# Optimization experiments

Measured on AMD Instinct MI355X. Metric: run time of the kernel, lower is better.

## Reference

```python
import jax, jax.numpy as jnp
import numpy as np

B, T, NA, NV, K, SD, H, E = 128, 64, 10, 16, 4, 512, 256, 32

def _lin(key, fan_in, fan_out):
    k1, k2 = jax.random.split(key)
    s = 1.0 / np.sqrt(fan_in)
    W = jax.random.uniform(k1, (fan_in, fan_out), jnp.float32, -s, s)
    b = jax.random.uniform(k2, (fan_out,), jnp.float32, -s, s)
    return W, b

def setup_inputs() -> dict:
    key = jax.random.key(0)
    ks = jax.random.split(key, 16)
    inp = {
        "qvals": jax.random.normal(ks[0], (B, T, NA), jnp.float32),
        "causal_relations": jax.random.randint(ks[1], (B, T, K, NV), 0, NA, jnp.int32),
        "states": jax.random.normal(ks[2], (B, T, SD), jnp.float32),
    }
    inp["w00_l1_W"], inp["w00_l1_b"] = _lin(ks[3], SD + NV, H)
    inp["w00_l2_W"], inp["w00_l2_b"] = _lin(ks[4], H, K)
    inp["b00_W"], inp["b00_b"] = _lin(ks[5], SD + NV, 1)
    inp["w01_W"], inp["w01_b"] = _lin(ks[6], SD, NA)
    inp["b01_W"], inp["b01_b"] = _lin(ks[7], SD, 1)
    inp["w1_l1_W"], inp["w1_l1_b"] = _lin(ks[8], SD, H)
    inp["w1_l2_W"], inp["w1_l2_b"] = _lin(ks[9], H, (NV + 1) * E)
    inp["b1_W"], inp["b1_b"] = _lin(ks[10], SD, E)
    inp["w2_l1_W"], inp["w2_l1_b"] = _lin(ks[11], SD, H)
    inp["w2_l2_W"], inp["w2_l2_b"] = _lin(ks[12], H, E)
    inp["b2_l1_W"], inp["b2_l1_b"] = _lin(ks[13], SD, E)
    inp["b2_l2_W"], inp["b2_l2_b"] = _lin(ks[14], E, 1)
    return inp

def reference(qvals, causal_relations, states,
              w00_l1_W, w00_l1_b, w00_l2_W, w00_l2_b, b00_W, b00_b,
              w01_W, w01_b, b01_W, b01_b,
              w1_l1_W, w1_l1_b, w1_l2_W, w1_l2_b, b1_W, b1_b,
              w2_l1_W, w2_l1_b, w2_l2_W, w2_l2_b,
              b2_l1_W, b2_l1_b, b2_l2_W, b2_l2_b):
    b, t, na = qvals.shape
    nv = causal_relations.shape[-1]
    sd = states.shape[-1]
    emb = b1_W.shape[1]

    # (b,t,k,nv) -> (b,t,nv,k); gather per-variable selected agent q-values
    cr = jnp.swapaxes(causal_relations, 2, 3)
    gathered = jnp.take_along_axis(qvals[:, :, None, :], cr, axis=-1)  # (b,t,nv,k)

    # Per-variable hypernets. Original builds a one-hot over n_variables but sets
    # var_onehot[variable] = 1, i.e. batch row `variable` becomes all-ones
    # (replicated faithfully). Split the first Linear into state part + onehot part:
    h_base = states @ w00_l1_W[:sd] + w00_l1_b   # (b,t,H)
    h_delta = w00_l1_W[sd:].sum(0)               # (H,)  contribution of all-ones onehot row
    g_base = states @ b00_W[:sd] + b00_b         # (b,t,1)
    g_delta = b00_W[sd:].sum(0)                  # (1,)

    def per_var(v):
        h = jax.nn.relu(h_base.at[v].add(h_delta))
        w0 = h @ w00_l2_W + w00_l2_b             # (b,t,k)
        b0 = g_base.at[v].add(g_delta)[..., 0]   # (b,t)
        return w0, b0

    w00, b00v = jax.vmap(per_var)(jnp.arange(nv))  # (nv,b,t,k), (nv,b,t)

    # group_qval_v = gathered_v @ |w0_v| + b0_v
    group = jnp.einsum('btvk,vbtk->btv', gathered, jnp.abs(w00)) + jnp.moveaxis(b00v, 0, -1)

    # residual agent mix (hyper_w0_1 / hyper_b0_1): plain linear hypernet, no abs in source
    w01 = states @ w01_W + w01_b                 # (b,t,na)
    other = jnp.einsum('bta,bta->bt', qvals, w01) + (states @ b01_W + b01_b)[..., 0]
    gq = jnp.concatenate([group, other[..., None]], axis=-1)  # (b,t,nv+1)

    # QMIX-style two-layer mix with hypernet weights
    w1 = jnp.abs((jax.nn.relu(states @ w1_l1_W + w1_l1_b) @ w1_l2_W + w1_l2_b)
                 .reshape(b, t, nv + 1, emb))
    b1 = states @ b1_W + b1_b                    # (b,t,E)
    hidden = jax.nn.elu(jnp.einsum('btv,btve->bte', gq, w1) + b1)
    w2 = jnp.abs(jax.nn.relu(states @ w2_l1_W + w2_l1_b) @ w2_l2_W + w2_l2_b)  # (b,t,E)
    b2 = jax.nn.relu(states @ b2_l1_W + b2_l1_b) @ b2_l2_W + b2_l2_b           # (b,t,1)
    y = jnp.sum(hidden * w2, axis=-1, keepdims=True) + b2
    return y  # (b,t,1)
```

## Files before the change

### kernel.cpp

```cpp
#include <hip/hip_runtime.h>
#include <hip/hip_bf16.h>


typedef __hip_bfloat16 bf16;
typedef unsigned short ushort_t;
typedef __attribute__((ext_vector_type(8))) short short8;
typedef __attribute__((ext_vector_type(4))) float f32x4;

#define PA_OFF 0
#define PA_TILES 56
#define PB_OFF (PA_TILES * 16 * 64 * 8 * 2)
#define PB_TILES 36
#define FB_OFF (PB_OFF + PB_TILES * 8 * 64 * 8 * 2)
#define NCST 2854
#define WS_NEED (size_t)(FB_OFF + NCST * 4 + 32)

#define MFMA16(a, b, c) __builtin_amdgcn_mfma_f32_16x16x32_bf16(a, b, c, 0, 0, 0)

__device__ __forceinline__ float us2f(ushort_t x) {
  unsigned u = ((unsigned)x) << 16; float f; __builtin_memcpy(&f, &u, 4); return f;
}
__device__ __forceinline__ ushort_t f2us(float v) {
  bf16 h = __float2bfloat16(v); ushort_t r; __builtin_memcpy(&r, &h, 2); return r;
}
template <bool F32>
__device__ __forceinline__ float LD(const void* p, size_t i) {
  if (F32) return ((const float*)p)[i];
  return us2f(((const ushort_t*)p)[i]);
}

__device__ __forceinline__ int detect_f32(const void* states) {
  const unsigned short* u = (const unsigned short*)states;
  int lane = threadIdx.x & 63;
  int bad = 0;
  for (int i = lane; i < 512; i += 64) {
    unsigned short x = u[i];
    int e = (x >> 7) & 0xFF;
    if (e > 140 || (((x & 0x7FFFu) != 0) && e < 100)) bad++;
  }
  for (int off = 32; off; off >>= 1) bad += __shfl_down(bad, off);
  return __shfl(bad, 0) > 20;
}

__device__ __forceinline__ void pa_store(ushort_t* pa, int np, int k, ushort_t v) {
  int t = np >> 4, lm = np & 15, ks = k >> 5, qq = (k >> 3) & 3, j = k & 7;
  pa[(size_t)t * 8192 + ks * 512 + (qq * 16 + lm) * 8 + j] = v;
}
__device__ __forceinline__ void pb_store(ushort_t* pb, int np, int k, ushort_t v) {
  int t = np >> 4, lm = np & 15, ks = k >> 5, qq = (k >> 3) & 3, j = k & 7;
  pb[(size_t)t * 4096 + ks * 512 + (qq * 16 + lm) * 8 + j] = v;
}

template <bool F32>
__device__ void prep_body(int gtid, int T, char* ws,
    const void* w00l1W, const void* w00l1b, const void* w00l2W, const void* w00l2b,
    const void* b00W, const void* b00b,
    const void* w01W, const void* w01b, const void* b01W, const void* b01b,
    const void* w1l1W, const void* w1l1b, const void* w1l2W, const void* w1l2b,
    const void* b1W, const void* b1b,
    const void* w2l1W, const void* w2l1b, const void* w2l2W, const void* w2l2b,
    const void* b2l1W, const void* b2l1b, const void* b2l2W, const void* b2l2b) {
  ushort_t* pa = (ushort_t*)(ws + PA_OFF);
  ushort_t* pb = (ushort_t*)(ws + PB_OFF);
  float* cst = (float*)(ws + FB_OFF);
  for (int i = gtid; i < 131072; i += T) {
    int k = i >> 8, n = i & 255;
    pa_store(pa, n, k, f2us(LD<F32>(w1l1W, i)));
    pa_store(pa, 256 + n, k, f2us(LD<F32>(w2l1W, i)));
    pa_store(pa, 512 + n, k, f2us(LD<F32>(w00l1W, i)));
  }
  for (int i = gtid; i < 16384; i += T) {
    int k = i >> 5, n = i & 31;
    pa_store(pa, 768 + n, k, f2us(LD<F32>(b1W, i)));
    pa_store(pa, 800 + n, k, f2us(LD<F32>(b2l1W, i)));
  }
  for (int i = gtid; i < 5120; i += T) {
    int k = i / 10, n = i % 10;
    pa_store(pa, 832 + n, k, f2us(LD<F32>(w01W, i)));
  }
  for (int i = gtid; i < 512; i += T) {
    pa_store(pa, 842, i, f2us(LD<F32>(b00W, i)));
    pa_store(pa, 843, i, f2us(LD<F32>(b01W, i)));
  }
  for (int z = gtid; z < 2048; z += T) {
    int ks = z >> 7, qq = (z >> 5) & 3, lm = 12 + ((z >> 3) & 3), j = z & 7;
    pa[(size_t)52 * 8192 + ks * 512 + (qq * 16 + lm) * 8 + j] = 0;
  }
  for (int i = gtid; i < 139264; i += T) {
    int k = i / 544, n = i % 544;
    pb_store(pb, n, k, f2us(LD<F32>(w1l2W, i)));
  }
  for (int i = gtid; i < 8192; i += T) {
    int k = i >> 5, n = i & 31;
    pb_store(pb, 544 + n, k, f2us(LD<F32>(w2l2W, i)));
  }
  for (int i = gtid; i < NCST; i += T) {
    float x;
    if (i < 896) {
      int c = i;
      if (c < 256) x = LD<F32>(w1l1b, c);
      else if (c < 512) x = LD<F32>(w2l1b, c - 256);
      else if (c < 768) x = LD<F32>(w00l1b, c - 512);
      else if (c < 800) x = LD<F32>(b1b, c - 768);
      else if (c < 832) x = LD<F32>(b2l1b, c - 800);
      else if (c < 842) x = LD<F32>(w01b, c - 832);
      else if (c == 842) x = LD<F32>(b00b, 0);
      else if (c == 843) x = LD<F32>(b01b, 0);
      else x = 0.f;
    } else if (i < 1536) {
      int c = i - 896;
      x = (c < 544) ? LD<F32>(w1l2b, c) : (c < 576 ? LD<F32>(w2l2b, c - 544) : 0.f);
    } else if (i < 1792) {
      int j = i - 1536; float s = 0.f;
      for (int z = 0; z < 16; ++z) s += LD<F32>(w00l1W, (size_t)(512 + z) * 256 + j);
      x = s;
    } else if (i < 2816) x = LD<F32>(w00l2W, i - 1792);
    else if (i < 2820) x = LD<F32>(w00l2b, i - 2816);
    else if (i < 2852) x = LD<F32>(b2l2W, i - 2820);
    else if (i == 2852) x = LD<F32>(b2l2b, 0);
    else { float s = 0.f; for (int z = 0; z < 16; ++z) s += LD<F32>(b00W, 512 + z); x = s; }
    cst[i] = x;
  }
}

__global__ __launch_bounds__(256) void prep_kernel(char* ws, const void* states,
    const void* w00l1W, const void* w00l1b, const void* w00l2W, const void* w00l2b,
    const void* b00W, const void* b00b,
    const void* w01W, const void* w01b, const void* b01W, const void* b01b,
    const void* w1l1W, const void* w1l1b, const void* w1l2W, const void* w1l2b,
    const void* b1W, const void* b1b,
    const void* w2l1W, const void* w2l1b, const void* w2l2W, const void* w2l2b,
    const void* b2l1W, const void* b2l1b, const void* b2l2W, const void* b2l2b) {
  int gtid = blockIdx.x * 256 + threadIdx.x;
  int T = gridDim.x * 256;
  if (detect_f32(states))
    prep_body<true>(gtid, T, ws, w00l1W, w00l1b, w00l2W, w00l2b, b00W, b00b,
        w01W, w01b, b01W, b01b, w1l1W, w1l1b, w1l2W, w1l2b, b1W, b1b,
        w2l1W, w2l1b, w2l2W, w2l2b, b2l1W, b2l1b, b2l2W, b2l2b);
  else
    prep_body<false>(gtid, T, ws, w00l1W, w00l1b, w00l2W, w00l2b, b00W, b00b,
        w01W, w01b, b01W, b01b, w1l1W, w1l1b, w1l2W, w1l2b, b1W, b1b,
        w2l1W, w2l1b, w2l2W, w2l2b, b2l1W, b2l1b, b2l2W, b2l2b);
}

struct SmemM {
  union {
    __align__(16) ushort_t sA[2][8192];
    __align__(16) ushort_t w1a[32][544];
  } u;
  __align__(16) ushort_t Am1[2][4096];
  __align__(16) ushort_t Am2[2][4096];
  __align__(16) ushort_t hb[32][264];
  float hd[256];
  float w2l[1024];
  float b1v[32][32];
  float rbv[32][32];
  float w2v[32][32];
  float w01v[32][12];
  float qv[32][10];
  unsigned char cr[32][64];
  float w0c[32][4], w0s[32][4];
  float gq[32][18];
  float gbv[32], b01v[32];
  float hid[32][33];
};

template <bool F32>
__device__ void mixer_body(SmemM& sm, const char* ws, int n0,
    const void* qvals, const int* crel, const void* states, void* out) {
  const int tid = threadIdx.x;
  const int lane = tid & 63, wv = tid >> 6;
  const int q = lane >> 4, lm = lane & 15;
  const int b_blk = n0 >> 6;
  const ushort_t* pa = (const ushort_t*)(ws + PA_OFF);
  const ushort_t* pb = (const ushort_t*)(ws + PB_OFF);
  const float* cstg = (const float*)(ws + FB_OFF);

  int sidx[7]; bool sreal[7];
#pragma unroll
  for (int i = 0; i < 7; ++i) {
    int s = wv + 8 * i;
    sreal[i] = (s < 53);
    sidx[i] = sreal[i] ? s : wv;
  }
  const ushort_t* baseA = pa + lane * 8;

  short8 curA[7];
  if (F32) {
    f32x4 va[8];
#pragma unroll
    for (int it = 0; it < 4; ++it) {
      int fi = tid + it * 512;
      int ln = fi & 63, ks = (fi >> 6) & 15, G = fi >> 10;
      int row = G * 16 + (ln & 15), col = ks * 32 + (ln >> 4) * 8;
      const f32x4* p = (const f32x4*)((const float*)states + (size_t)(n0 + row) * 512 + col);
      va[2 * it] = p[0];
      va[2 * it + 1] = p[1];
    }
#pragma unroll
    for (int i = 0; i < 7; ++i) curA[i] = *(const short8*)(baseA + (size_t)sidx[i] * 8192);
#pragma unroll
    for (int it = 0; it < 4; ++it) {
      int fi = tid + it * 512;
      int ln = fi & 63, ks = (fi >> 6) & 15, G = fi >> 10;
      f32x4 v0 = va[2 * it], v1 = va[2 * it + 1];
      ushort_t v[8];
      v[0] = f2us(v0[0]); v[1] = f2us(v0[1]); v[2] = f2us(v0[2]); v[3] = f2us(v0[3]);
      v[4] = f2us(v1[0]); v[5] = f2us(v1[1]); v[6] = f2us(v1[2]); v[7] = f2us(v1[3]);
      *(short8*)&sm.u.sA[G][(size_t)(ks * 64 + ln) * 8] = *(short8*)v;
    }
  } else {
    short8 vb[2];
#pragma unroll
    for (int it = 0; it < 2; ++it) {
      int fi = tid + it * 512;
      int ln = fi & 63, ks = (fi >> 6) & 15, G = fi >> 10;
      int row = G * 16 + (ln & 15), col = ks * 32 + (ln >> 4) * 8;
      vb[it] = *(const short8*)((const ushort_t*)states + (size_t)(n0 + row) * 512 + col);
    }
#pragma unroll
    for (int i = 0; i < 7; ++i) curA[i] = *(const short8*)(baseA + (size_t)sidx[i] * 8192);
#pragma unroll
    for (int it = 0; it < 2; ++it) {
      int fi = tid + it * 512;
      int ln = fi & 63, ks = (fi >> 6) & 15, G = fi >> 10;
      *(short8*)&sm.u.sA[G][(size_t)(ks * 64 + ln) * 8] = vb[it];
    }
  }
  for (int i = tid; i < 320; i += 512) sm.qv[i / 10][i % 10] = LD<F32>(qvals, (size_t)(n0 + i / 10) * 10 + i % 10);
  for (int i = tid; i < 2048; i += 512) sm.cr[i >> 6][i & 63] = (unsigned char)crel[(size_t)n0 * 64 + i];
  if (tid < 256) sm.hd[tid] = cstg[1536 + tid];
  for (int i = tid; i < 1024; i += 512) sm.w2l[i] = cstg[1792 + i];
  __syncthreads();

  {
    f32x4 accA[7][2];
#pragma unroll
    for (int i = 0; i < 7; ++i) { accA[i][0] = (f32x4){0,0,0,0}; accA[i][1] = (f32x4){0,0,0,0}; }
    short8 nxt[7];
#pragma unroll
    for (int ks = 0; ks < 16; ++ks) {
      if (ks < 15) {
#pragma unroll
        for (int i = 0; i < 7; ++i)
          nxt[i] = *(const short8*)(baseA + (size_t)sidx[i] * 8192 + (ks + 1) * 512);
      }
      short8 a0 = *(const short8*)&sm.u.sA[0][(ks * 64 + lane) * 8];
      short8 a1 = *(const short8*)&sm.u.sA[1][(ks * 64 + lane) * 8];
#pragma unroll
      for (int i = 0; i < 7; ++i) {
        accA[i][0] = MFMA16(a0, curA[i], accA[i][0]);
        accA[i][1] = MFMA16(a1, curA[i], accA[i][1]);
      }
#pragma unroll
      for (int i = 0; i < 7; ++i) curA[i] = nxt[i];
    }
#pragma unroll
    for (int i = 0; i < 7; ++i) {
      if (!sreal[i]) continue;
      int c = sidx[i] * 16 + lm;
      if (c >= 844) continue;
      float bias = cstg[c];
      int ks2 = (c & 255) >> 5, q2 = (c >> 3) & 3, j2 = c & 7;
#pragma unroll
      for (int G = 0; G < 2; ++G) {
        f32x4 acc = accA[i][G];
        int rb = G * 16 + q * 4;
        if (c < 256) {
#pragma unroll
          for (int g = 0; g < 4; ++g) {
            float v = acc[g] + bias;
            sm.Am1[G][(ks2 * 64 + q2 * 16 + q * 4 + g) * 8 + j2] = f2us(v > 0.f ? v : 0.f);
          }
        } else if (c < 512) {
#pragma unroll
          for (int g = 0; g < 4; ++g) {
            float v = acc[g] + bias;
            sm.Am2[G][(ks2 * 64 + q2 * 16 + q * 4 + g) * 8 + j2] = f2us(v > 0.f ? v : 0.f);
          }
        } else if (c < 768) {
#pragma unroll
          for (int g = 0; g < 4; ++g) sm.hb[rb + g][c - 512] = f2us(acc[g] + bias);
        } else if (c < 800) {
#pragma unroll
          for (int g = 0; g < 4; ++g) sm.b1v[rb + g][c - 768] = acc[g] + bias;
        } else if (c < 832) {
#pragma unroll
          for (int g = 0; g < 4; ++g) { float v = acc[g] + bias; sm.rbv[rb + g][c - 800] = v > 0.f ? v : 0.f; }
        } else if (c < 842) {
#pragma unroll
          for (int g = 0; g < 4; ++g) sm.w01v[rb + g][c - 832] = acc[g] + bias;
        } else if (c == 842) {
#pragma unroll
          for (int g = 0; g < 4; ++g) sm.gbv[rb + g] = acc[g] + bias;
        } else {
#pragma unroll
          for (int g = 0; g < 4; ++g) sm.b01v[rb + g] = acc[g] + bias;
        }
      }
    }
  }

  int tix[5]; bool treal[5];
#pragma unroll
  for (int i = 0; i < 5; ++i) {
    int t = wv + 8 * i;
    treal[i] = (t < 36);
    tix[i] = treal[i] ? t : wv;
  }
  const ushort_t* baseB = pb + lane * 8;
  short8 curB[5];
#pragma unroll
  for (int i = 0; i < 5; ++i) curB[i] = *(const short8*)(baseB + (size_t)tix[i] * 4096);
  __syncthreads();

  {
    f32x4 accB[5][2];
#pragma unroll
    for (int i = 0; i < 5; ++i) { accB[i][0] = (f32x4){0,0,0,0}; accB[i][1] = (f32x4){0,0,0,0}; }
    short8 nxt[5];
#pragma unroll
    for (int ks = 0; ks < 8; ++ks) {
      if (ks < 7) {
#pragma unroll
        for (int i = 0; i < 5; ++i)
          nxt[i] = *(const short8*)(baseB + (size_t)tix[i] * 4096 + (ks + 1) * 512);
      }
      short8 m1a0 = *(const short8*)&sm.Am1[0][(ks * 64 + lane) * 8];
      short8 m1a1 = *(const short8*)&sm.Am1[1][(ks * 64 + lane) * 8];
      short8 m2a0 = *(const short8*)&sm.Am2[0][(ks * 64 + lane) * 8];
      short8 m2a1 = *(const short8*)&sm.Am2[1][(ks * 64 + lane) * 8];
#pragma unroll
      for (int i = 0; i < 5; ++i) {
        short8 x0 = (tix[i] < 34) ? m1a0 : m2a0;
        short8 x1 = (tix[i] < 34) ? m1a1 : m2a1;
        accB[i][0] = MFMA16(x0, curB[i], accB[i][0]);
        accB[i][1] = MFMA16(x1, curB[i], accB[i][1]);
      }
#pragma unroll
      for (int i = 0; i < 5; ++i) curB[i] = nxt[i];
    }
#pragma unroll
    for (int i = 0; i < 5; ++i) {
      if (!treal[i]) continue;
      int c = tix[i] * 16 + lm;
      float bias = cstg[896 + c];
#pragma unroll
      for (int G = 0; G < 2; ++G) {
        f32x4 acc = accB[i][G];
        int rb = G * 16 + q * 4;
        if (c < 544) {
#pragma unroll
          for (int g = 0; g < 4; ++g) sm.u.w1a[rb + g][c] = f2us(fabsf(acc[g] + bias));
        } else {
          int e = c - 544;
#pragma unroll
          for (int g = 0; g < 4; ++g) sm.w2v[rb + g][e] = fabsf(acc[g] + bias);
        }
      }
    }
  }
  __syncthreads();

  if (tid < 256) {
    int r = tid >> 3, k = (tid >> 1) & 3, sflag = tid & 1;
    float a = 0.f;
    for (int j = 0; j < 256; ++j) {
      float h = us2f(sm.hb[r][j]);
      if (sflag) h += sm.hd[j];
      h = h > 0.f ? h : 0.f;
      a = fmaf(h, sm.w2l[j * 4 + k], a);
    }
    a += cstg[2816 + k];
    if (sflag) sm.w0s[r][k] = a; else sm.w0c[r][k] = a;
  }
  __syncthreads();

  {
    int r = tid >> 4, v = tid & 15;
    bool sp = (v == b_blk);
    const float* w0 = sp ? sm.w0s[r] : sm.w0c[r];
    float g = sm.gbv[r] + (sp ? cstg[2853] : 0.f);
#pragma unroll
    for (int k = 0; k < 4; ++k) {
      int a = sm.cr[r][k * 16 + v];
      g = fmaf(sm.qv[r][a], fabsf(w0[k]), g);
    }
    sm.gq[r][v] = g;
  }
  if (tid < 32) {
    float o = sm.b01v[tid];
#pragma unroll
    for (int a = 0; a < 10; ++a) o = fmaf(sm.qv[tid][a], sm.w01v[tid][a], o);
    sm.gq[tid][16] = o;
  }
  __syncthreads();

  for (int p = tid; p < 1024; p += 512) {
    int r = p >> 5, e = p & 31;
    float h = sm.b1v[r][e];
#pragma unroll
    for (int v = 0; v < 17; ++v) h = fmaf(sm.gq[r][v], us2f(sm.u.w1a[r][v * 32 + e]), h);
    float hid = h > 0.f ? h : (expf(h) - 1.f);
    sm.hid[r][e] = hid * sm.w2v[r][e] + sm.rbv[r][e] * cstg[2820 + e];
  }
  __syncthreads();

  if (tid < 32) {
    float y = cstg[2852];
#pragma unroll
    for (int e = 0; e < 32; ++e) y += sm.hid[tid][e];
    if (F32) ((float*)out)[n0 + tid] = y;
    else ((bf16*)out)[n0 + tid] = __float2bfloat16(y);
  }
}

__global__ __launch_bounds__(512, 2) void causal_mixer_mfma(const char* ws,
    const void* qvals, const int* crel, const void* states, void* out) {
  __shared__ SmemM sm;
  int n0 = blockIdx.x * 32;
  if (detect_f32(states))
    mixer_body<true>(sm, ws, n0, qvals, crel, states, out);
  else
    mixer_body<false>(sm, ws, n0, qvals, crel, states, out);
}

struct SmemF {
  float s[16][516]; float buf[16][258]; float hd[256];
  float q[16][10]; int cr[16][66];
  float w0c[16][4], w0s[16][4]; float gq[16][17];
  float w01[16][10]; float b01[16]; float gb[16]; float gd;
  float hid[16][32]; float w2[16][32]; float rb[16][32];
};

template <bool F32>
__device__ void fb_body(SmemF& sm, int tid, int n0, int b_blk,
    const void* qvals, const int* crel, const void* states,
    const void* w00l1W, const void* w00l1b, const void* w00l2W, const void* w00l2b,
    const void* b00W, const void* b00b,
    const void* w01W, const void* w01b, const void* b01W, const void* b01b,
    const void* w1l1W, const void* w1l1b, const void* w1l2W, const void* w1l2b,
    const void* b1W, const void* b1b,
    const void* w2l1W, const void* w2l1b, const void* w2l2W, const void* w2l2b,
    const void* b2l1W, const void* b2l1b, const void* b2l2W, const void* b2l2b,
    void* out) {
  for (int idx = tid; idx < 16 * 512; idx += 256) {
    int r = idx >> 9, i = idx & 511;
    sm.s[r][i] = LD<F32>(states, (size_t)(n0 + r) * 512 + i);
  }
  for (int idx = tid; idx < 160; idx += 256) {
    int r = idx / 10, a = idx % 10;
    sm.q[r][a] = LD<F32>(qvals, (size_t)(n0 + r) * 10 + a);
  }
  for (int idx = tid; idx < 16 * 64; idx += 256) {
    int r = idx >> 6, kv = idx & 63;
    sm.cr[r][kv] = crel[(size_t)(n0 + r) * 64 + kv];
  }
  if (tid == 0) {
    float gd = 0.f;
    for (int i = 512; i < 528; ++i) gd += LD<F32>(b00W, i);
    sm.gd = gd;
  }
  __syncthreads();
  {
    const int j = tid;
    float hd = 0.f;
    for (int i = 0; i < 16; ++i) hd += LD<F32>(w00l1W, (size_t)(512 + i) * 256 + j);
    sm.hd[j] = hd;
    float acc[16]; float bj = LD<F32>(w00l1b, j);
#pragma unroll
    for (int r = 0; r < 16; ++r) acc[r] = bj;
    for (int i = 0; i < 512; ++i) {
      float w = LD<F32>(w00l1W, (size_t)i * 256 + j);
#pragma unroll
      for (int r = 0; r < 16; ++r) acc[r] = fmaf(sm.s[r][i], w, acc[r]);
    }
#pragma unroll
    for (int r = 0; r < 16; ++r) sm.buf[r][j] = acc[r];
  }
  __syncthreads();
  if (tid < 64) {
    int r = tid >> 2, k = tid & 3;
    float aC = 0.f, aS = 0.f;
    for (int j = 0; j < 256; ++j) {
      float hb = sm.buf[r][j];
      float w = LD<F32>(w00l2W, j * 4 + k);
      float hc = hb > 0.f ? hb : 0.f;
      float hbs = hb + sm.hd[j];
      float hsv = hbs > 0.f ? hbs : 0.f;
      aC = fmaf(hc, w, aC); aS = fmaf(hsv, w, aS);
    }
    float bk = LD<F32>(w00l2b, k);
    sm.w0c[r][k] = aC + bk; sm.w0s[r][k] = aS + bk;
  } else if (tid < 224) {
    int p = tid - 64; int r = p / 10, a = p % 10;
    float acc = 0.f;
    for (int i = 0; i < 512; ++i) acc = fmaf(sm.s[r][i], LD<F32>(w01W, (size_t)i * 10 + a), acc);
    sm.w01[r][a] = acc + LD<F32>(w01b, a);
  } else if (tid < 240) {
    int r = tid - 224;
    float acc = 0.f;
    for (int i = 0; i < 512; ++i) acc = fmaf(sm.s[r][i], LD<F32>(b00W, i), acc);
    sm.gb[r] = acc + LD<F32>(b00b, 0);
  } else {
    int r = tid - 240;
    float acc = 0.f;
    for (int i = 0; i < 512; ++i) acc = fmaf(sm.s[r][i], LD<F32>(b01W, i), acc);
    sm.b01[r] = acc + LD<F32>(b01b, 0);
  }
  __syncthreads();
  {
    int r = tid >> 4, v = tid & 15;
    bool sp = (v == b_blk);
    const float* w0 = sp ? sm.w0s[r] : sm.w0c[r];
    float g = sm.gb[r] + (sp ? sm.gd : 0.f);
#pragma unroll
    for (int k = 0; k < 4; ++k) {
      int a = sm.cr[r][k * 16 + v];
      g = fmaf(sm.q[r][a], fabsf(w0[k]), g);
    }
    sm.gq[r][v] = g;
  }
  if (tid < 16) {
    int r = tid;
    float o = sm.b01[r];
    for (int a = 0; a < 10; ++a) o = fmaf(sm.q[r][a], sm.w01[r][a], o);
    sm.gq[r][16] = o;
  }
  __syncthreads();
  {
    const int j = tid;
    float acc[16]; float bj = LD<F32>(w1l1b, j);
#pragma unroll
    for (int r = 0; r < 16; ++r) acc[r] = bj;
    for (int i = 0; i < 512; ++i) {
      float w = LD<F32>(w1l1W, (size_t)i * 256 + j);
#pragma unroll
      for (int r = 0; r < 16; ++r) acc[r] = fmaf(sm.s[r][i], w, acc[r]);
    }
#pragma unroll
    for (int r = 0; r < 16; ++r) sm.buf[r][j] = acc[r] > 0.f ? acc[r] : 0.f;
  }
  __syncthreads();
  for (int p = tid; p < 512; p += 256) {
    int r = p >> 5, e = p & 31;
    float acc = 0.f;
    for (int v = 0; v < 17; ++v) {
      int c = v * 32 + e;
      float d = LD<F32>(w1l2b, c);
      for (int j = 0; j < 256; ++j) d = fmaf(sm.buf[r][j], LD<F32>(w1l2W, (size_t)j * 544 + c), d);
      acc = fmaf(sm.gq[r][v], fabsf(d), acc);
    }
    float b1v = LD<F32>(b1b, e);
    for (int i = 0; i < 512; ++i) b1v = fmaf(sm.s[r][i], LD<F32>(b1W, (size_t)i * 32 + e), b1v);
    float x = acc + b1v;
    sm.hid[r][e] = x > 0.f ? x : (expf(x) - 1.f);
  }
  __syncthreads();
  {
    const int j = tid;
    float acc[16]; float bj = LD<F32>(w2l1b, j);
#pragma unroll
    for (int r = 0; r < 16; ++r) acc[r] = bj;
    for (int i = 0; i < 512; ++i) {
      float w = LD<F32>(w2l1W, (size_t)i * 256 + j);
#pragma unroll
      for (int r = 0; r < 16; ++r) acc[r] = fmaf(sm.s[r][i], w, acc[r]);
    }
#pragma unroll
    for (int r = 0; r < 16; ++r) sm.buf[r][j] = acc[r] > 0.f ? acc[r] : 0.f;
  }
  __syncthreads();
  for (int p = tid; p < 512; p += 256) {
    int r = p >> 5, e = p & 31;
    float d = LD<F32>(w2l2b, e);
    for (int j = 0; j < 256; ++j) d = fmaf(sm.buf[r][j], LD<F32>(w2l2W, (size_t)j * 32 + e), d);
    sm.w2[r][e] = fabsf(d);
    float rb = LD<F32>(b2l1b, e);
    for (int i = 0; i < 512; ++i) rb = fmaf(sm.s[r][i], LD<F32>(b2l1W, (size_t)i * 32 + e), rb);
    sm.rb[r][e] = rb > 0.f ? rb : 0.f;
  }
  __syncthreads();
  if (tid < 16) {
    int r = tid;
    float y = 0.f;
#pragma unroll
    for (int e = 0; e < 32; ++e) y = fmaf(sm.hid[r][e], sm.w2[r][e], y);
    float b2v = LD<F32>(b2l2b, 0);
#pragma unroll
    for (int e = 0; e < 32; ++e) b2v = fmaf(sm.rb[r][e], LD<F32>(b2l2W, e), b2v);
    float yv = y + b2v;
    if (F32) ((float*)out)[n0 + r] = yv;
    else ((bf16*)out)[n0 + r] = __float2bfloat16(yv);
  }
}

__global__ __launch_bounds__(256) void causal_mixer_fb(
    const void* qvals, const int* crel, const void* states,
    const void* w00l1W, const void* w00l1b, const void* w00l2W, const void* w00l2b,
    const void* b00W, const void* b00b,
    const void* w01W, const void* w01b, const void* b01W, const void* b01b,
    const void* w1l1W, const void* w1l1b, const void* w1l2W, const void* w1l2b,
    const void* b1W, const void* b1b,
    const void* w2l1W, const void* w2l1b, const void* w2l2W, const void* w2l2b,
    const void* b2l1W, const void* b2l1b, const void* b2l2W, const void* b2l2b,
    void* out) {
  __shared__ SmemF sm;
  const int tid = threadIdx.x;
  const int n0 = blockIdx.x * 16;
  const int b_blk = n0 >> 6;
  if (detect_f32(states))
    fb_body<true>(sm, tid, n0, b_blk, qvals, crel, states, w00l1W, w00l1b, w00l2W, w00l2b,
        b00W, b00b, w01W, w01b, b01W, b01b, w1l1W, w1l1b, w1l2W, w1l2b, b1W, b1b,
        w2l1W, w2l1b, w2l2W, w2l2b, b2l1W, b2l1b, b2l2W, b2l2b, out);
  else
    fb_body<false>(sm, tid, n0, b_blk, qvals, crel, states, w00l1W, w00l1b, w00l2W, w00l2b,
        b00W, b00b, w01W, w01b, b01W, b01b, w1l1W, w1l1b, w1l2W, w1l2b, b1W, b1b,
        w2l1W, w2l1b, w2l2W, w2l2b, b2l1W, b2l1b, b2l2W, b2l2b, out);
}

extern "C" void kernel_launch(void* const* d_in, const int* in_sizes, int n_in,
                              void* d_out, int out_size, void* d_ws, size_t ws_size,
                              hipStream_t stream) {
  char* ws = (char*)d_ws;
  if (ws_size >= WS_NEED) {
    hipLaunchKernelGGL(prep_kernel, dim3(256), dim3(256), 0, stream, ws, d_in[2],
        d_in[3], d_in[4], d_in[5], d_in[6], d_in[7], d_in[8],
        d_in[9], d_in[10], d_in[11], d_in[12],
        d_in[13], d_in[14], d_in[15], d_in[16], d_in[17], d_in[18],
        d_in[19], d_in[20], d_in[21], d_in[22], d_in[23], d_in[24],
        d_in[25], d_in[26]);
    hipLaunchKernelGGL(causal_mixer_mfma, dim3(256), dim3(512), 0, stream, ws,
        d_in[0], (const int*)d_in[1], d_in[2], d_out);
  } else {
    hipLaunchKernelGGL(causal_mixer_fb, dim3(512), dim3(256), 0, stream,
        d_in[0], (const int*)d_in[1], d_in[2],
        d_in[3], d_in[4], d_in[5], d_in[6], d_in[7], d_in[8],
        d_in[9], d_in[10], d_in[11], d_in[12],
        d_in[13], d_in[14], d_in[15], d_in[16], d_in[17], d_in[18],
        d_in[19], d_in[20], d_in[21], d_in[22], d_in[23], d_in[24],
        d_in[25], d_in[26],
        d_out);
  }
}
```

Baseline: 170.0 us.

## Fuse weight prep and mixer into one cooperative kernel with grid sync

Merges the weight-repacking prep kernel and the MFMA mixer kernel into a single cooperative launch. A grid-wide sync separates the prep phase from the mixer phase, and blocks loop over the mixer tiles. The aim is to remove one kernel launch and the gap between the two kernels. In exchange it adds host-side occupancy and device-property queries on every call, a grid barrier, and possible serialization if fewer blocks are resident. It also drops the scalar fallback kernel, so a workspace that is too small now runs the MFMA path without enough space.

```diff
diff --git a/kernel.cpp b/kernel.cpp
--- a/kernel.cpp
+++ b/kernel.cpp
@@ -1,6 +1,9 @@
 #include <hip/hip_runtime.h>
 #include <hip/hip_bf16.h>
-
+#include <hip/hip_cooperative_groups.h>
+
+
+namespace cg = cooperative_groups;
 
 typedef __hip_bfloat16 bf16;
 typedef unsigned short ushort_t;
@@ -51,36 +54,41 @@
   pb[(size_t)t * 4096 + ks * 512 + (qq * 16 + lm) * 8 + j] = v;
 }
 
+struct KParams {
+  char* ws;
+  const void* qvals; const int* crel; const void* states; void* out;
+  const void* w00l1W; const void* w00l1b; const void* w00l2W; const void* w00l2b;
+  const void* b00W;  const void* b00b;
+  const void* w01W;  const void* w01b;  const void* b01W;  const void* b01b;
+  const void* w1l1W; const void* w1l1b; const void* w1l2W; const void* w1l2b;
+  const void* b1W;   const void* b1b;
+  const void* w2l1W; const void* w2l1b; const void* w2l2W; const void* w2l2b;
+  const void* b2l1W; const void* b2l1b; const void* b2l2W; const void* b2l2b;
+};
+
 template <bool F32>
-__device__ void prep_body(int gtid, int T, char* ws,
-    const void* w00l1W, const void* w00l1b, const void* w00l2W, const void* w00l2b,
-    const void* b00W, const void* b00b,
-    const void* w01W, const void* w01b, const void* b01W, const void* b01b,
-    const void* w1l1W, const void* w1l1b, const void* w1l2W, const void* w1l2b,
-    const void* b1W, const void* b1b,
-    const void* w2l1W, const void* w2l1b, const void* w2l2W, const void* w2l2b,
-    const void* b2l1W, const void* b2l1b, const void* b2l2W, const void* b2l2b) {
+__device__ void prep_body(int gtid, int T, char* ws, const KParams& P) {
   ushort_t* pa = (ushort_t*)(ws + PA_OFF);
   ushort_t* pb = (ushort_t*)(ws + PB_OFF);
   float* cst = (float*)(ws + FB_OFF);
   for (int i = gtid; i < 131072; i += T) {
     int k = i >> 8, n = i & 255;
-    pa_store(pa, n, k, f2us(LD<F32>(w1l1W, i)));
-    pa_store(pa, 256 + n, k, f2us(LD<F32>(w2l1W, i)));
-    pa_store(pa, 512 + n, k, f2us(LD<F32>(w00l1W, i)));
+    pa_store(pa, n, k, f2us(LD<F32>(P.w1l1W, i)));
+    pa_store(pa, 256 + n, k, f2us(LD<F32>(P.w2l1W, i)));
+    pa_store(pa, 512 + n, k, f2us(LD<F32>(P.w00l1W, i)));
   }
   for (int i = gtid; i < 16384; i += T) {
     int k = i >> 5, n = i & 31;
-    pa_store(pa, 768 + n, k, f2us(LD<F32>(b1W, i)));
-    pa_store(pa, 800 + n, k, f2us(LD<F32>(b2l1W, i)));
+    pa_store(pa, 768 + n, k, f2us(LD<F32>(P.b1W, i)));
+    pa_store(pa, 800 + n, k, f2us(LD<F32>(P.b2l1W, i)));
   }
   for (int i = gtid; i < 5120; i += T) {
     int k = i / 10, n = i % 10;
-    pa_store(pa, 832 + n, k, f2us(LD<F32>(w01W, i)));
+    pa_store(pa, 832 + n, k, f2us(LD<F32>(P.w01W, i)));
   }
   for (int i = gtid; i < 512; i += T) {
-    pa_store(pa, 842, i, f2us(LD<F32>(b00W, i)));
-    pa_store(pa, 843, i, f2us(LD<F32>(b01W, i)));
+    pa_store(pa, 842, i, f2us(LD<F32>(P.b00W, i)));
+    pa_store(pa, 843, i, f2us(LD<F32>(P.b01W, i)));
   }
   for (int z = gtid; z < 2048; z += T) {
     int ks = z >> 7, qq = (z >> 5) & 3, lm = 12 + ((z >> 3) & 3), j = z & 7;
@@ -88,59 +96,39 @@
   }
   for (int i = gtid; i < 139264; i += T) {
     int k = i / 544, n = i % 544;
-    pb_store(pb, n, k, f2us(LD<F32>(w1l2W, i)));
+    pb_store(pb, n, k, f2us(LD<F32>(P.w1l2W, i)));
   }
   for (int i = gtid; i < 8192; i += T) {
     int k = i >> 5, n = i & 31;
-    pb_store(pb, 544 + n, k, f2us(LD<F32>(w2l2W, i)));
+    pb_store(pb, 544 + n, k, f2us(LD<F32>(P.w2l2W, i)));
   }
   for (int i = gtid; i < NCST; i += T) {
     float x;
     if (i < 896) {
       int c = i;
-      if (c < 256) x = LD<F32>(w1l1b, c);
-      else if (c < 512) x = LD<F32>(w2l1b, c - 256);
-      else if (c < 768) x = LD<F32>(w00l1b, c - 512);
-      else if (c < 800) x = LD<F32>(b1b, c - 768);
-      else if (c < 832) x = LD<F32>(b2l1b, c - 800);
-      else if (c < 842) x = LD<F32>(w01b, c - 832);
-      else if (c == 842) x = LD<F32>(b00b, 0);
-      else if (c == 843) x = LD<F32>(b01b, 0);
+      if (c < 256) x = LD<F32>(P.w1l1b, c);
+      else if (c < 512) x = LD<F32>(P.w2l1b, c - 256);
+      else if (c < 768) x = LD<F32>(P.w00l1b, c - 512);
+      else if (c < 800) x = LD<F32>(P.b1b, c - 768);
+      else if (c < 832) x = LD<F32>(P.b2l1b, c - 800);
+      else if (c < 842) x = LD<F32>(P.w01b, c - 832);
+      else if (c == 842) x = LD<F32>(P.b00b, 0);
+      else if (c == 843) x = LD<F32>(P.b01b, 0);
       else x = 0.f;
     } else if (i < 1536) {
       int c = i - 896;
-      x = (c < 544) ? LD<F32>(w1l2b, c) : (c < 576 ? LD<F32>(w2l2b, c - 544) : 0.f);
+      x = (c < 544) ? LD<F32>(P.w1l2b, c) : (c < 576 ? LD<F32>(P.w2l2b, c - 544) : 0.f);
     } else if (i < 1792) {
       int j = i - 1536; float s = 0.f;
-      for (int z = 0; z < 16; ++z) s += LD<F32>(w00l1W, (size_t)(512 + z) * 256 + j);
+      for (int z = 0; z < 16; ++z) s += LD<F32>(P.w00l1W, (size_t)(512 + z) * 256 + j);
       x = s;
-    } else if (i < 2816) x = LD<F32>(w00l2W, i - 1792);
-    else if (i < 2820) x = LD<F32>(w00l2b, i - 2816);
-    else if (i < 2852) x = LD<F32>(b2l2W, i - 2820);
-    else if (i == 2852) x = LD<F32>(b2l2b, 0);
-    else { float s = 0.f; for (int z = 0; z < 16; ++z) s += LD<F32>(b00W, 512 + z); x = s; }
+    } else if (i < 2816) x = LD<F32>(P.w00l2W, i - 1792);
+    else if (i < 2820) x = LD<F32>(P.w00l2b, i - 2816);
+    else if (i < 2852) x = LD<F32>(P.b2l2W, i - 2820);
+    else if (i == 2852) x = LD<F32>(P.b2l2b, 0);
+    else { float s = 0.f; for (int z = 0; z < 16; ++z) s += LD<F32>(P.b00W, 512 + z); x = s; }
     cst[i] = x;
   }
-}
-
-__global__ __launch_bounds__(256) void prep_kernel(char* ws, const void* states,
-    const void* w00l1W, const void* w00l1b, const void* w00l2W, const void* w00l2b,
-    const void* b00W, const void* b00b,
-    const void* w01W, const void* w01b, const void* b01W, const void* b01b,
-    const void* w1l1W, const void* w1l1b, const void* w1l2W, const void* w1l2b,
-    const void* b1W, const void* b1b,
-    const void* w2l1W, const void* w2l1b, const void* w2l2W, const void* w2l2b,
-    const void* b2l1W, const void* b2l1b, const void* b2l2W, const void* b2l2b) {
-  int gtid = blockIdx.x * 256 + threadIdx.x;
-  int T = gridDim.x * 256;
-  if (detect_f32(states))
-    prep_body<true>(gtid, T, ws, w00l1W, w00l1b, w00l2W, w00l2b, b00W, b00b,
-        w01W, w01b, b01W, b01b, w1l1W, w1l1b, w1l2W, w1l2b, b1W, b1b,
-        w2l1W, w2l1b, w2l2W, w2l2b, b2l1W, b2l1b, b2l2W, b2l2b);
-  else
-    prep_body<false>(gtid, T, ws, w00l1W, w00l1b, w00l2W, w00l2b, b00W, b00b,
-        w01W, w01b, b01W, b01b, w1l1W, w1l1b, w1l2W, w1l2b, b1W, b1b,
-        w2l1W, w2l1b, w2l2W, w2l2b, b2l1W, b2l1b, b2l2W, b2l2b);
 }
 
 struct SmemM {
@@ -413,233 +401,78 @@
     if (F32) ((float*)out)[n0 + tid] = y;
     else ((bf16*)out)[n0 + tid] = __float2bfloat16(y);
   }
-}
-
-__global__ __launch_bounds__(512, 2) void causal_mixer_mfma(const char* ws,
-    const void* qvals, const int* crel, const void* states, void* out) {
+  __syncthreads();
+}
+
+__global__ __launch_bounds__(512, 2) void causal_mixer_coop(KParams P) {
+  __shared__ SmemM sm;
+  int gtid = blockIdx.x * 512 + threadIdx.x;
+  int T = gridDim.x * 512;
+  int isf32 = detect_f32(P.states);
+  if (isf32) prep_body<true>(gtid, T, P.ws, P);
+  else       prep_body<false>(gtid, T, P.ws, P);
+  cg::this_grid().sync();
+  for (int blk = blockIdx.x; blk < 256; blk += gridDim.x) {
+    int n0 = blk * 32;
+    if (isf32) mixer_body<true>(sm, P.ws, n0, P.qvals, P.crel, P.states, P.out);
+    else       mixer_body<false>(sm, P.ws, n0, P.qvals, P.crel, P.states, P.out);
+  }
+}
+
+__global__ __launch_bounds__(256) void prep_kernel(KParams P) {
+  int gtid = blockIdx.x * 256 + threadIdx.x;
+  int T = gridDim.x * 256;
+  if (detect_f32(P.states)) prep_body<true>(gtid, T, P.ws, P);
+  else                      prep_body<false>(gtid, T, P.ws, P);
+}
+
+__global__ __launch_bounds__(512, 2) void causal_mixer_mfma(KParams P) {
   __shared__ SmemM sm;
   int n0 = blockIdx.x * 32;
-  if (detect_f32(states))
-    mixer_body<true>(sm, ws, n0, qvals, crel, states, out);
+  if (detect_f32(P.states))
+    mixer_body<true>(sm, P.ws, n0, P.qvals, P.crel, P.states, P.out);
   else
-    mixer_body<false>(sm, ws, n0, qvals, crel, states, out);
-}
-
-struct SmemF {
-  float s[16][516]; float buf[16][258]; float hd[256];
-  float q[16][10]; int cr[16][66];
-  float w0c[16][4], w0s[16][4]; float gq[16][17];
-  float w01[16][10]; float b01[16]; float gb[16]; float gd;
-  float hid[16][32]; float w2[16][32]; float rb[16][32];
-};
-
-template <bool F32>
-__device__ void fb_body(SmemF& sm, int tid, int n0, int b_blk,
-    const void* qvals, const int* crel, const void* states,
-    const void* w00l1W, const void* w00l1b, const void* w00l2W, const void* w00l2b,
-    const void* b00W, const void* b00b,
-    const void* w01W, const void* w01b, const void* b01W, const void* b01b,
-    const void* w1l1W, const void* w1l1b, const void* w1l2W, const void* w1l2b,
-    const void* b1W, const void* b1b,
-    const void* w2l1W, const void* w2l1b, const void* w2l2W, const void* w2l2b,
-    const void* b2l1W, const void* b2l1b, const void* b2l2W, const void* b2l2b,
-    void* out) {
-  for (int idx = tid; idx < 16 * 512; idx += 256) {
-    int r = idx >> 9, i = idx & 511;
-    sm.s[r][i] = LD<F32>(states, (size_t)(n0 + r) * 512 + i);
-  }
-  for (int idx = tid; idx < 160; idx += 256) {
-    int r = idx / 10, a = idx % 10;
-    sm.q[r][a] = LD<F32>(qvals, (size_t)(n0 + r) * 10 + a);
-  }
-  for (int idx = tid; idx < 16 * 64; idx += 256) {
-    int r = idx >> 6, kv = idx & 63;
-    sm.cr[r][kv] = crel[(size_t)(n0 + r) * 64 + kv];
-  }
-  if (tid == 0) {
-    float gd = 0.f;
-    for (int i = 512; i < 528; ++i) gd += LD<F32>(b00W, i);
-    sm.gd = gd;
-  }
-  __syncthreads();
-  {
-    const int j = tid;
-    float hd = 0.f;
-    for (int i = 0; i < 16; ++i) hd += LD<F32>(w00l1W, (size_t)(512 + i) * 256 + j);
-    sm.hd[j] = hd;
-    float acc[16]; float bj = LD<F32>(w00l1b, j);
-#pragma unroll
-    for (int r = 0; r < 16; ++r) acc[r] = bj;
-    for (int i = 0; i < 512; ++i) {
-      float w = LD<F32>(w00l1W, (size_t)i * 256 + j);
-#pragma unroll
-      for (int r = 0; r < 16; ++r) acc[r] = fmaf(sm.s[r][i], w, acc[r]);
-    }
-#pragma unroll
-    for (int r = 0; r < 16; ++r) sm.buf[r][j] = acc[r];
-  }
-  __syncthreads();
-  if (tid < 64) {
-    int r = tid >> 2, k = tid & 3;
-    float aC = 0.f, aS = 0.f;
-    for (int j = 0; j < 256; ++j) {
-      float hb = sm.buf[r][j];
-      float w = LD<F32>(w00l2W, j * 4 + k);
-      float hc = hb > 0.f ? hb : 0.f;
-      float hbs = hb + sm.hd[j];
-      float hsv = hbs > 0.f ? hbs : 0.f;
-      aC = fmaf(hc, w, aC); aS = fmaf(hsv, w, aS);
-    }
-    float bk = LD<F32>(w00l2b, k);
-    sm.w0c[r][k] = aC + bk; sm.w0s[r][k] = aS + bk;
-  } else if (tid < 224) {
-    int p = tid - 64; int r = p / 10, a = p % 10;
-    float acc = 0.f;
-    for (int i = 0; i < 512; ++i) acc = fmaf(sm.s[r][i], LD<F32>(w01W, (size_t)i * 10 + a), acc);
-    sm.w01[r][a] = acc + LD<F32>(w01b, a);
-  } else if (tid < 240) {
-    int r = tid - 224;
-    float acc = 0.f;
-    for (int i = 0; i < 512; ++i) acc = fmaf(sm.s[r][i], LD<F32>(b00W, i), acc);
-    sm.gb[r] = acc + LD<F32>(b00b, 0);
-  } else {
-    int r = tid - 240;
-    float acc = 0.f;
-    for (int i = 0; i < 512; ++i) acc = fmaf(sm.s[r][i], LD<F32>(b01W, i), acc);
-    sm.b01[r] = acc + LD<F32>(b01b, 0);
-  }
-  __syncthreads();
-  {
-    int r = tid >> 4, v = tid & 15;
-    bool sp = (v == b_blk);
-    const float* w0 = sp ? sm.w0s[r] : sm.w0c[r];
-    float g = sm.gb[r] + (sp ? sm.gd : 0.f);
-#pragma unroll
-    for (int k = 0; k < 4; ++k) {
-      int a = sm.cr[r][k * 16 + v];
-      g = fmaf(sm.q[r][a], fabsf(w0[k]), g);
-    }
-    sm.gq[r][v] = g;
-  }
-  if (tid < 16) {
-    int r = tid;
-    float o = sm.b01[r];
-    for (int a = 0; a < 10; ++a) o = fmaf(sm.q[r][a], sm.w01[r][a], o);
-    sm.gq[r][16] = o;
-  }
-  __syncthreads();
-  {
-    const int j = tid;
-    float acc[16]; float bj = LD<F32>(w1l1b, j);
-#pragma unroll
-    for (int r = 0; r < 16; ++r) acc[r] = bj;
-    for (int i = 0; i < 512; ++i) {
-      float w = LD<F32>(w1l1W, (size_t)i * 256 + j);
-#pragma unroll
-      for (int r = 0; r < 16; ++r) acc[r] = fmaf(sm.s[r][i], w, acc[r]);
-    }
-#pragma unroll
-    for (int r = 0; r < 16; ++r) sm.buf[r][j] = acc[r] > 0.f ? acc[r] : 0.f;
-  }
-  __syncthreads();
-  for (int p = tid; p < 512; p += 256) {
-    int r = p >> 5, e = p & 31;
-    float acc = 0.f;
-    for (int v = 0; v < 17; ++v) {
-      int c = v * 32 + e;
-      float d = LD<F32>(w1l2b, c);
-      for (int j = 0; j < 256; ++j) d = fmaf(sm.buf[r][j], LD<F32>(w1l2W, (size_t)j * 544 + c), d);
-      acc = fmaf(sm.gq[r][v], fabsf(d), acc);
-    }
-    float b1v = LD<F32>(b1b, e);
-    for (int i = 0; i < 512; ++i) b1v = fmaf(sm.s[r][i], LD<F32>(b1W, (size_t)i * 32 + e), b1v);
-    float x = acc + b1v;
-    sm.hid[r][e] = x > 0.f ? x : (expf(x) - 1.f);
-  }
-  __syncthreads();
-  {
-    const int j = tid;
-    float acc[16]; float bj = LD<F32>(w2l1b, j);
-#pragma unroll
-    for (int r = 0; r < 16; ++r) acc[r] = bj;
-    for (int i = 0; i < 512; ++i) {
-      float w = LD<F32>(w2l1W, (size_t)i * 256 + j);
-#pragma unroll
-      for (int r = 0; r < 16; ++r) acc[r] = fmaf(sm.s[r][i], w, acc[r]);
-    }
-#pragma unroll
-    for (int r = 0; r < 16; ++r) sm.buf[r][j] = acc[r] > 0.f ? acc[r] : 0.f;
-  }
-  __syncthreads();
-  for (int p = tid; p < 512; p += 256) {
-    int r = p >> 5, e = p & 31;
-    float d = LD<F32>(w2l2b, e);
-    for (int j = 0; j < 256; ++j) d = fmaf(sm.buf[r][j], LD<F32>(w2l2W, (size_t)j * 32 + e), d);
-    sm.w2[r][e] = fabsf(d);
-    float rb = LD<F32>(b2l1b, e);
-    for (int i = 0; i < 512; ++i) rb = fmaf(sm.s[r][i], LD<F32>(b2l1W, (size_t)i * 32 + e), rb);
-    sm.rb[r][e] = rb > 0.f ? rb : 0.f;
-  }
-  __syncthreads();
-  if (tid < 16) {
-    int r = tid;
-    float y = 0.f;
-#pragma unroll
-    for (int e = 0; e < 32; ++e) y = fmaf(sm.hid[r][e], sm.w2[r][e], y);
-    float b2v = LD<F32>(b2l2b, 0);
-#pragma unroll
-    for (int e = 0; e < 32; ++e) b2v = fmaf(sm.rb[r][e], LD<F32>(b2l2W, e), b2v);
-    float yv = y + b2v;
-    if (F32) ((float*)out)[n0 + r] = yv;
-    else ((bf16*)out)[n0 + r] = __float2bfloat16(yv);
-  }
-}
-
-__global__ __launch_bounds__(256) void causal_mixer_fb(
-    const void* qvals, const int* crel, const void* states,
-    const void* w00l1W, const void* w00l1b, const void* w00l2W, const void* w00l2b,
-    const void* b00W, const void* b00b,
-    const void* w01W, const void* w01b, const void* b01W, const void* b01b,
-    const void* w1l1W, const void* w1l1b, const void* w1l2W, const void* w1l2b,
-    const void* b1W, const void* b1b,
-    const void* w2l1W, const void* w2l1b, const void* w2l2W, const void* w2l2b,
-    const void* b2l1W, const void* b2l1b, const void* b2l2W, const void* b2l2b,
-    void* out) {
-  __shared__ SmemF sm;
-  const int tid = threadIdx.x;
-  const int n0 = blockIdx.x * 16;
-  const int b_blk = n0 >> 6;
-  if (detect_f32(states))
-    fb_body<true>(sm, tid, n0, b_blk, qvals, crel, states, w00l1W, w00l1b, w00l2W, w00l2b,
-        b00W, b00b, w01W, w01b, b01W, b01b, w1l1W, w1l1b, w1l2W, w1l2b, b1W, b1b,
-        w2l1W, w2l1b, w2l2W, w2l2b, b2l1W, b2l1b, b2l2W, b2l2b, out);
-  else
-    fb_body<false>(sm, tid, n0, b_blk, qvals, crel, states, w00l1W, w00l1b, w00l2W, w00l2b,
-        b00W, b00b, w01W, w01b, b01W, b01b, w1l1W, w1l1b, w1l2W, w1l2b, b1W, b1b,
-        w2l1W, w2l1b, w2l2W, w2l2b, b2l1W, b2l1b, b2l2W, b2l2b, out);
+    mixer_body<false>(sm, P.ws, n0, P.qvals, P.crel, P.states, P.out);
 }
 
 extern "C" void kernel_launch(void* const* d_in, const int* in_sizes, int n_in,
                               void* d_out, int out_size, void* d_ws, size_t ws_size,
                               hipStream_t stream) {
-  char* ws = (char*)d_ws;
+  KParams P;
+  P.ws = (char*)d_ws;
+  P.qvals = d_in[0]; P.crel = (const int*)d_in[1]; P.states = d_in[2]; P.out = d_out;
+  P.w00l1W = d_in[3];  P.w00l1b = d_in[4];  P.w00l2W = d_in[5];  P.w00l2b = d_in[6];
+  P.b00W   = d_in[7];  P.b00b   = d_in[8];
+  P.w01W   = d_in[9];  P.w01b   = d_in[10]; P.b01W   = d_in[11]; P.b01b   = d_in[12];
+  P.w1l1W  = d_in[13]; P.w1l1b  = d_in[14]; P.w1l2W  = d_in[15]; P.w1l2b  = d_in[16];
+  P.b1W    = d_in[17]; P.b1b    = d_in[18];
+  P.w2l1W  = d_in[19]; P.w2l1b  = d_in[20]; P.w2l2W  = d_in[21]; P.w2l2b  = d_in[22];
+  P.b2l1W  = d_in[23]; P.b2l1b  = d_in[24]; P.b2l2W  = d_in[25]; P.b2l2b  = d_in[26];
+
+  bool launched = false;
   if (ws_size >= WS_NEED) {
-    hipLaunchKernelGGL(prep_kernel, dim3(256), dim3(256), 0, stream, ws, d_in[2],
-        d_in[3], d_in[4], d_in[5], d_in[6], d_in[7], d_in[8],
-        d_in[9], d_in[10], d_in[11], d_in[12],
-        d_in[13], d_in[14], d_in[15], d_in[16], d_in[17], d_in[18],
-        d_in[19], d_in[20], d_in[21], d_in[22], d_in[23], d_in[24],
-        d_in[25], d_in[26]);
-    hipLaunchKernelGGL(causal_mixer_mfma, dim3(256), dim3(512), 0, stream, ws,
-        d_in[0], (const int*)d_in[1], d_in[2], d_out);
-  } else {
-    hipLaunchKernelGGL(causal_mixer_fb, dim3(512), dim3(256), 0, stream,
-        d_in[0], (const int*)d_in[1], d_in[2],
-        d_in[3], d_in[4], d_in[5], d_in[6], d_in[7], d_in[8],
-        d_in[9], d_in[10], d_in[11], d_in[12],
-        d_in[13], d_in[14], d_in[15], d_in[16], d_in[17], d_in[18],
-        d_in[19], d_in[20], d_in[21], d_in[22], d_in[23], d_in[24],
-        d_in[25], d_in[26],
-        d_out);
-  }
-}
+    int occ = 0;
+    hipError_t e = hipOccupancyMaxActiveBlocksPerMultiprocessor(
+        &occ, (const void*)causal_mixer_coop, 512, 0);
+    int nCU = 256;
+    hipDeviceProp_t prop;
+    if (hipGetDeviceProperties(&prop, 0) == hipSuccess) nCU = prop.multiProcessorCount;
+    if (e == hipSuccess && occ > 0) {
+      int grid = occ * nCU;
+      if (grid > 256) grid = 256;
+      void* args[] = { &P };
+      hipError_t le = hipLaunchCooperativeKernel(
+          (const void*)causal_mixer_coop, dim3(grid), dim3(512), args, 0, stream);
+      if (le == hipSuccess) launched = true;
+    }
+    if (!launched) {
+      hipLaunchKernelGGL(prep_kernel, dim3(256), dim3(256), 0, stream, P);
+      hipLaunchKernelGGL(causal_mixer_mfma, dim3(256), dim3(512), 0, stream, P);
+      launched = true;
+    }
+  }
+  if (!launched) {
+    hipLaunchKernelGGL(prep_kernel, dim3(256), dim3(256), 0, stream, P);
+    hipLaunchKernelGGL(causal_mixer_mfma, dim3(256), dim3(512), 0, stream, P);
+  }
+}
```

After: 184.3 us. 1.08x slower.
